# Kernel optimization log

Measured on AMD Instinct MI355X. Metric: run time of the kernel, lower is better.

The kernel has to match this reference:

```python
import jax, jax.numpy as jnp
import numpy as np
jax.config.update("jax_enable_x64", True)

T, C, F = 2048, 2048, 8192
f32 = jnp.float32
f64 = jnp.float64


def setup_inputs() -> dict:
    key = jax.random.key(0)
    ks = jax.random.split(key, 20)
    s = 0.02
    return {
        "x": jax.random.normal(ks[0], (T, C), f32),
        "att_shift": jnp.zeros((C,), f32),
        "wkv_state": jnp.zeros((2, C), f32),
        "ffn_shift": jnp.zeros((C,), f32),
        "ln1_w": jnp.ones((C,), f32),
        "ln1_b": jnp.zeros((C,), f32),
        "ln2_w": jnp.ones((C,), f32),
        "ln2_b": jnp.zeros((C,), f32),
        "time_mix_k": jax.random.uniform(ks[1], (C,), f32),
        "time_mix_v": jax.random.uniform(ks[2], (C,), f32),
        "time_mix_r": jax.random.uniform(ks[3], (C,), f32),
        "time_decay": jax.random.normal(ks[4], (C,), f32) * 0.5,
        "time_first": jax.random.normal(ks[5], (C,), f32) * 0.5,
        "att_key": jax.random.normal(ks[6], (C, C), f32) * s,
        "att_value": jax.random.normal(ks[7], (C, C), f32) * s,
        "att_receptance": jax.random.normal(ks[8], (C, C), f32) * s,
        "att_output": jax.random.normal(ks[9], (C, C), f32) * s,
        "ffn_time_mix_k": jax.random.uniform(ks[10], (C,), f32),
        "ffn_time_mix_r": jax.random.uniform(ks[11], (C,), f32),
        "ffn_key": jax.random.normal(ks[12], (F, C), f32) * s,
        "ffn_value": jax.random.normal(ks[13], (C, F), f32) * s,
        "ffn_receptance": jax.random.normal(ks[14], (C, C), f32) * s,
    }


def _ln(x, w, b):
    m = x.mean(-1, keepdims=True)
    v = x.var(-1, keepdims=True)
    return (x - m) * jax.lax.rsqrt(v + 1e-5) * w + b


def _wkv(time_decay, time_first, k, v, wkv_state):
    # faithful to wkv_mop: double-precision math, float32 state round-trip per step
    u = time_first.astype(f64)
    w = -jnp.exp(time_decay.astype(f64))
    ew = jnp.exp(w)

    def step(carry, kv_t):
        a, b = carry  # float32 states [C]
        k_t, v_t = kv_t
        kd = k_t.astype(f64)
        vd = v_t.astype(f64)
        e = jnp.exp(u + w + kd)
        y = (a + e * vd) / (b + e)
        kk = jnp.exp(kd)
        a2 = ((a + kk * vd) * ew).astype(f32)
        b2 = ((b + kk) * ew).astype(f32)
        return (a2, b2), y.astype(f32)

    _, y = jax.lax.scan(step, (wkv_state[0], wkv_state[1]), (k, v))
    return y  # [T, C]


def reference(x, att_shift, wkv_state, ffn_shift, ln1_w, ln1_b, ln2_w, ln2_b,
              time_mix_k, time_mix_v, time_mix_r, time_decay, time_first,
              att_key, att_value, att_receptance, att_output,
              ffn_time_mix_k, ffn_time_mix_r, ffn_key, ffn_value, ffn_receptance):
    # --- TimeMix (att) on rx = ln1(x); shiftamount=2 -> prev token of rx ---
    rx = _ln(x, ln1_w, ln1_b)                         # [T, C]
    xx = jnp.concatenate([att_shift[None, :], rx[:-1]], axis=0)
    xk = rx * time_mix_k + xx * (1.0 - time_mix_k)
    xv = rx * time_mix_v + xx * (1.0 - time_mix_v)
    xr = rx * time_mix_r + xx * (1.0 - time_mix_r)
    k = xk @ att_key.T                                # [T, C]
    v = xv @ att_value.T
    sr = jax.nn.sigmoid(xr @ att_receptance.T)
    y = _wkv(time_decay, time_first, k, v, wkv_state)
    x = x + (sr * y) @ att_output.T
    # --- ChannelMix (ffn) on fx = ln2(x); shift = prev token of fx ---
    fx = _ln(x, ln2_w, ln2_b)
    fxx = jnp.concatenate([ffn_shift[None, :], fx[:-1]], axis=0)
    fk = fx * ffn_time_mix_k + fxx * (1.0 - ffn_time_mix_k)
    fr = fx * ffn_time_mix_r + fxx * (1.0 - ffn_time_mix_r)
    kf = jnp.square(jax.nn.relu(fk @ ffn_key.T))      # [T, F]
    kv = kf @ ffn_value.T                             # [T, C]
    out = x + jax.nn.sigmoid(fr @ ffn_receptance.T) * kv
    return out
```

## Files before the change

kernel.cpp:

```cpp
#include <hip/hip_runtime.h>
#include <hip/hip_bf16.h>

typedef unsigned short u16;
typedef short bf16x8 __attribute__((ext_vector_type(8)));
typedef float f32x4 __attribute__((ext_vector_type(4)));

#define T_DIM 2048
#define C_DIM 2048
#define F_DIM 8192
#define WKV_L 32
#define WKV_P (T_DIM / WKV_L)

__device__ __forceinline__ u16 f2bf(float f) {
    unsigned int u = __float_as_uint(f);
    u += 0x7fff + ((u >> 16) & 1);
    return (u16)(u >> 16);
}

__device__ __forceinline__ void async16(const void* g, void* l) {
    __builtin_amdgcn_global_load_lds(
        (__attribute__((address_space(1))) const unsigned int*)g,
        (__attribute__((address_space(3))) unsigned int*)l, 16, 0, 0);
}

__global__ __launch_bounds__(256) void ln_mix3(
        const float* __restrict__ x, const float* __restrict__ sh,
        const float* __restrict__ w, const float* __restrict__ b,
        const float* __restrict__ mk, const float* __restrict__ mv,
        const float* __restrict__ mr,
        u16* __restrict__ xk, u16* __restrict__ xv, u16* __restrict__ xr) {
    __shared__ float red[16];
    const int t = blockIdx.x, tid = threadIdx.x;
    const float4* cr = (const float4*)(x + (size_t)t * C_DIM);
    float4 c0 = cr[tid * 2], c1 = cr[tid * 2 + 1];
    float s = c0.x + c0.y + c0.z + c0.w + c1.x + c1.y + c1.z + c1.w;
    float q = c0.x * c0.x + c0.y * c0.y + c0.z * c0.z + c0.w * c0.w
            + c1.x * c1.x + c1.y * c1.y + c1.z * c1.z + c1.w * c1.w;
    float4 p0, p1;
    float sp = 0.f, qp = 0.f;
    if (t > 0) {
        const float4* pr = (const float4*)(x + (size_t)(t - 1) * C_DIM);
        p0 = pr[tid * 2]; p1 = pr[tid * 2 + 1];
        sp = p0.x + p0.y + p0.z + p0.w + p1.x + p1.y + p1.z + p1.w;
        qp = p0.x * p0.x + p0.y * p0.y + p0.z * p0.z + p0.w * p0.w
           + p1.x * p1.x + p1.y * p1.y + p1.z * p1.z + p1.w * p1.w;
    } else {
        const float4* pr = (const float4*)sh;
        p0 = pr[tid * 2]; p1 = pr[tid * 2 + 1];
    }
    #pragma unroll
    for (int off = 32; off > 0; off >>= 1) {
        s += __shfl_down(s, off);   q += __shfl_down(q, off);
        sp += __shfl_down(sp, off); qp += __shfl_down(qp, off);
    }
    const int lane = tid & 63, wv = tid >> 6;
    if (lane == 0) { red[wv] = s; red[4 + wv] = q; red[8 + wv] = sp; red[12 + wv] = qp; }
    __syncthreads();
    if (tid == 0) {
        red[0] += red[1] + red[2] + red[3];
        red[4] += red[5] + red[6] + red[7];
        red[8] += red[9] + red[10] + red[11];
        red[12] += red[13] + red[14] + red[15];
    }
    __syncthreads();
    const float mc = red[0] * (1.f / C_DIM);
    const float ic = rsqrtf(red[4] * (1.f / C_DIM) - mc * mc + 1e-5f);
    const float mp = red[8] * (1.f / C_DIM);
    const float ip = rsqrtf(red[12] * (1.f / C_DIM) - mp * mp + 1e-5f);
    const float4* w4 = (const float4*)w;
    const float4* b4 = (const float4*)b;
    #pragma unroll
    for (int j = 0; j < 2; ++j) {
        const int i4 = tid * 2 + j;
        float4 cv = j ? c1 : c0, pv = j ? p1 : p0;
        float4 wv4 = w4[i4], bv = b4[i4];
        float4 cl, pl;
        cl.x = (cv.x - mc) * ic * wv4.x + bv.x;
        cl.y = (cv.y - mc) * ic * wv4.y + bv.y;
        cl.z = (cv.z - mc) * ic * wv4.z + bv.z;
        cl.w = (cv.w - mc) * ic * wv4.w + bv.w;
        if (t > 0) {
            pl.x = (pv.x - mp) * ip * wv4.x + bv.x;
            pl.y = (pv.y - mp) * ip * wv4.y + bv.y;
            pl.z = (pv.z - mp) * ip * wv4.z + bv.z;
            pl.w = (pv.w - mp) * ip * wv4.w + bv.w;
        } else pl = pv;
        const size_t o = (size_t)t * (C_DIM / 4) + i4;
        float4 m;
        ushort4 r;
        m = ((const float4*)mk)[i4];
        r.x = f2bf(cl.x * m.x + pl.x * (1.f - m.x));
        r.y = f2bf(cl.y * m.y + pl.y * (1.f - m.y));
        r.z = f2bf(cl.z * m.z + pl.z * (1.f - m.z));
        r.w = f2bf(cl.w * m.w + pl.w * (1.f - m.w));
        ((ushort4*)xk)[o] = r;
        m = ((const float4*)mv)[i4];
        r.x = f2bf(cl.x * m.x + pl.x * (1.f - m.x));
        r.y = f2bf(cl.y * m.y + pl.y * (1.f - m.y));
        r.z = f2bf(cl.z * m.z + pl.z * (1.f - m.z));
        r.w = f2bf(cl.w * m.w + pl.w * (1.f - m.w));
        ((ushort4*)xv)[o] = r;
        m = ((const float4*)mr)[i4];
        r.x = f2bf(cl.x * m.x + pl.x * (1.f - m.x));
        r.y = f2bf(cl.y * m.y + pl.y * (1.f - m.y));
        r.z = f2bf(cl.z * m.z + pl.z * (1.f - m.z));
        r.w = f2bf(cl.w * m.w + pl.w * (1.f - m.w));
        ((ushort4*)xr)[o] = r;
    }
}

__global__ __launch_bounds__(256) void ln_mix2(
        const float* __restrict__ x, const float* __restrict__ sh,
        const float* __restrict__ w, const float* __restrict__ b,
        const float* __restrict__ mk, const float* __restrict__ mr,
        u16* __restrict__ fk, u16* __restrict__ fr) {
    __shared__ float red[16];
    const int t = blockIdx.x, tid = threadIdx.x;
    const float4* cr = (const float4*)(x + (size_t)t * C_DIM);
    float4 c0 = cr[tid * 2], c1 = cr[tid * 2 + 1];
    float s = c0.x + c0.y + c0.z + c0.w + c1.x + c1.y + c1.z + c1.w;
    float q = c0.x * c0.x + c0.y * c0.y + c0.z * c0.z + c0.w * c0.w
            + c1.x * c1.x + c1.y * c1.y + c1.z * c1.z + c1.w * c1.w;
    float4 p0, p1;
    float sp = 0.f, qp = 0.f;
    if (t > 0) {
        const float4* pr = (const float4*)(x + (size_t)(t - 1) * C_DIM);
        p0 = pr[tid * 2]; p1 = pr[tid * 2 + 1];
        sp = p0.x + p0.y + p0.z + p0.w + p1.x + p1.y + p1.z + p1.w;
        qp = p0.x * p0.x + p0.y * p0.y + p0.z * p0.z + p0.w * p0.w
           + p1.x * p1.x + p1.y * p1.y + p1.z * p1.z + p1.w * p1.w;
    } else {
        const float4* pr = (const float4*)sh;
        p0 = pr[tid * 2]; p1 = pr[tid * 2 + 1];
    }
    #pragma unroll
    for (int off = 32; off > 0; off >>= 1) {
        s += __shfl_down(s, off);   q += __shfl_down(q, off);
        sp += __shfl_down(sp, off); qp += __shfl_down(qp, off);
    }
    const int lane = tid & 63, wv = tid >> 6;
    if (lane == 0) { red[wv] = s; red[4 + wv] = q; red[8 + wv] = sp; red[12 + wv] = qp; }
    __syncthreads();
    if (tid == 0) {
        red[0] += red[1] + red[2] + red[3];
        red[4] += red[5] + red[6] + red[7];
        red[8] += red[9] + red[10] + red[11];
        red[12] += red[13] + red[14] + red[15];
    }
    __syncthreads();
    const float mc = red[0] * (1.f / C_DIM);
    const float ic = rsqrtf(red[4] * (1.f / C_DIM) - mc * mc + 1e-5f);
    const float mp = red[8] * (1.f / C_DIM);
    const float ip = rsqrtf(red[12] * (1.f / C_DIM) - mp * mp + 1e-5f);
    const float4* w4 = (const float4*)w;
    const float4* b4 = (const float4*)b;
    #pragma unroll
    for (int j = 0; j < 2; ++j) {
        const int i4 = tid * 2 + j;
        float4 cv = j ? c1 : c0, pv = j ? p1 : p0;
        float4 wv4 = w4[i4], bv = b4[i4];
        float4 cl, pl;
        cl.x = (cv.x - mc) * ic * wv4.x + bv.x;
        cl.y = (cv.y - mc) * ic * wv4.y + bv.y;
        cl.z = (cv.z - mc) * ic * wv4.z + bv.z;
        cl.w = (cv.w - mc) * ic * wv4.w + bv.w;
        if (t > 0) {
            pl.x = (pv.x - mp) * ip * wv4.x + bv.x;
            pl.y = (pv.y - mp) * ip * wv4.y + bv.y;
            pl.z = (pv.z - mp) * ip * wv4.z + bv.z;
            pl.w = (pv.w - mp) * ip * wv4.w + bv.w;
        } else pl = pv;
        const size_t o = (size_t)t * (C_DIM / 4) + i4;
        float4 m;
        ushort4 r;
        m = ((const float4*)mk)[i4];
        r.x = f2bf(cl.x * m.x + pl.x * (1.f - m.x));
        r.y = f2bf(cl.y * m.y + pl.y * (1.f - m.y));
        r.z = f2bf(cl.z * m.z + pl.z * (1.f - m.z));
        r.w = f2bf(cl.w * m.w + pl.w * (1.f - m.w));
        ((ushort4*)fk)[o] = r;
        m = ((const float4*)mr)[i4];
        r.x = f2bf(cl.x * m.x + pl.x * (1.f - m.x));
        r.y = f2bf(cl.y * m.y + pl.y * (1.f - m.y));
        r.z = f2bf(cl.z * m.z + pl.z * (1.f - m.z));
        r.w = f2bf(cl.w * m.w + pl.w * (1.f - m.w));
        ((ushort4*)fr)[o] = r;
    }
}

__global__ __launch_bounds__(256) void cvt_bf16(const float* __restrict__ in,
                                                u16* __restrict__ out, int n8) {
    int i = blockIdx.x * 256 + threadIdx.x;
    const int stride = gridDim.x * 256;
    for (; i < n8; i += stride) {
        const float4* p = (const float4*)(in + (size_t)i * 8);
        float4 a = p[0], b = p[1];
        ushort4 lo, hi;
        lo.x = f2bf(a.x); lo.y = f2bf(a.y); lo.z = f2bf(a.z); lo.w = f2bf(a.w);
        hi.x = f2bf(b.x); hi.y = f2bf(b.y); hi.z = f2bf(b.z); hi.w = f2bf(b.w);
        ((ushort4*)out)[i * 2] = lo;
        ((ushort4*)out)[i * 2 + 1] = hi;
    }
}

__global__ __launch_bounds__(256) void cvt4_bf16(const float* __restrict__ i0,
                                                 const float* __restrict__ i1,
                                                 const float* __restrict__ i2,
                                                 const float* __restrict__ i3,
                                                 u16* __restrict__ out, int n8) {
    const int sel = blockIdx.y;
    const float* in = sel == 0 ? i0 : (sel == 1 ? i1 : (sel == 2 ? i2 : i3));
    u16* o = out + (size_t)sel * n8 * 8;
    int i = blockIdx.x * 256 + threadIdx.x;
    const int stride = gridDim.x * 256;
    for (; i < n8; i += stride) {
        const float4* p = (const float4*)(in + (size_t)i * 8);
        float4 a = p[0], b = p[1];
        ushort4 lo, hi;
        lo.x = f2bf(a.x); lo.y = f2bf(a.y); lo.z = f2bf(a.z); lo.w = f2bf(a.w);
        hi.x = f2bf(b.x); hi.y = f2bf(b.y); hi.z = f2bf(b.z); hi.w = f2bf(b.w);
        ((ushort4*)o)[i * 2] = lo;
        ((ushort4*)o)[i * 2 + 1] = hi;
    }
}

__global__ __launch_bounds__(256) void reduce4(const float* __restrict__ p0,
                                               const float* __restrict__ p1,
                                               const float* __restrict__ p2,
                                               const float* __restrict__ p3,
                                               float* __restrict__ o, int n4) {
    int i = blockIdx.x * 256 + threadIdx.x;
    const int stride = gridDim.x * 256;
    for (; i < n4; i += stride) {
        float4 a = ((const float4*)p0)[i], b = ((const float4*)p1)[i];
        float4 c = ((const float4*)p2)[i], d = ((const float4*)p3)[i];
        float4 r;
        r.x = a.x + b.x + c.x + d.x;
        r.y = a.y + b.y + c.y + d.y;
        r.z = a.z + b.z + c.z + d.z;
        r.w = a.w + b.w + c.w + d.w;
        ((float4*)o)[i] = r;
    }
}

__global__ __launch_bounds__(256) void wkv_part(const float* __restrict__ td,
                                                const float* __restrict__ k,
                                                const float* __restrict__ v,
                                                float* __restrict__ Ab,
                                                float* __restrict__ Bb) {
    const int idx = blockIdx.x * 256 + threadIdx.x;
    const int c = idx & (C_DIM - 1);
    const int p = idx >> 11;
    const float ew = expf(-expf(td[c]));
    float A = 0.f, B = 0.f;
    size_t o = (size_t)(p * WKV_L) * C_DIM + c;
    #pragma unroll 4
    for (int i = 0; i < WKV_L; ++i, o += C_DIM) {
        const float kk = expf(k[o]);
        A = (A + kk * v[o]) * ew;
        B = (B + kk) * ew;
    }
    Ab[p * C_DIM + c] = A;
    Bb[p * C_DIM + c] = B;
}

__global__ __launch_bounds__(256) void wkv_comb(const float* __restrict__ td,
                                                const float* __restrict__ st,
                                                const float* __restrict__ Ab,
                                                const float* __restrict__ Bb,
                                                float* __restrict__ Sa,
                                                float* __restrict__ Sb) {
    const int c = blockIdx.x * 256 + threadIdx.x;
    const float w = -expf(td[c]);
    const float dL = expf(w * (float)WKV_L);
    float a = st[c];
    float b = st[C_DIM + c];
    #pragma unroll 4
    for (int p = 0; p < WKV_P; ++p) {
        Sa[p * C_DIM + c] = a;
        Sb[p * C_DIM + c] = b;
        a = dL * a + Ab[p * C_DIM + c];
        b = dL * b + Bb[p * C_DIM + c];
    }
}

__global__ __launch_bounds__(256) void wkv_emit(const float* __restrict__ td,
                                                const float* __restrict__ tf,
                                                const float* __restrict__ k,
                                                const float* __restrict__ v,
                                                const float* __restrict__ r,
                                                const float* __restrict__ Sa,
                                                const float* __restrict__ Sb,
                                                u16* __restrict__ pout) {
    const int idx = blockIdx.x * 256 + threadIdx.x;
    const int c = idx & (C_DIM - 1);
    const int p = idx >> 11;
    const float u = tf[c];
    const float w = -expf(td[c]);
    const float ew = expf(w);
    float a = Sa[p * C_DIM + c];
    float b = Sb[p * C_DIM + c];
    size_t o = (size_t)(p * WKV_L) * C_DIM + c;
    #pragma unroll 2
    for (int i = 0; i < WKV_L; ++i, o += C_DIM) {
        const float kt = k[o], vt = v[o], rt = r[o];
        const float e = expf(u + w + kt);
        const float y = (a + e * vt) / (b + e);
        const float kk = expf(kt);
        a = (a + kk * vt) * ew;
        b = (b + kk) * ew;
        const float sr = 1.f / (1.f + expf(-rt));
        pout[o] = f2bf(sr * y);
    }
}

enum { EPI_F32 = 0, EPI_ADDX = 1, EPI_RELU2 = 2, EPI_SIGMULADD = 3 };

template <int EPI>
__global__ __launch_bounds__(256, 3) void gemm_bt(
        const u16* __restrict__ A, int lda, long a_zs,
        const u16* __restrict__ B, int ldb, long b_zs,
        long koff, int Kloop,
        void* __restrict__ outp, int ldo, long o_zs,
        const float* __restrict__ aux1, const float* __restrict__ aux2) {
    __shared__ u16 lds[3 * 8192];
    const int tid = threadIdx.x;
    const int l = tid & 63, w = tid >> 6;
    const int wr2 = w >> 1, wc2 = w & 1;

    const int gx = gridDim.x, gy = gridDim.y;
    const int nxy = gx * gy;
    const int flat = (blockIdx.z * gy + blockIdx.y) * gx + blockIdx.x;
    const int cpx = (nxy * gridDim.z) >> 3;
    const int swz = (flat & 7) * cpx + (flat >> 3);
    const int z = swz / nxy;
    const int rem = swz - z * nxy;
    const int bm = rem % gy;
    const int bn = rem / gy;

    const u16* Ag = A + (size_t)z * a_zs + (size_t)z * koff + (size_t)bm * 128 * lda;
    const u16* Bg = B + (size_t)z * b_zs + (size_t)z * koff + (size_t)bn * 128 * ldb;

    long gA[2], gB[2];
    int dA[2], dB[2];
    #pragma unroll
    for (int j = 0; j < 2; ++j) {
        const int off = j * 4096 + w * 1024 + l * 16;
        const int row = off >> 6;
        const int cb = (off & 63) ^ (((off >> 9) & 1) << 5);
        gA[j] = (long)row * lda + (cb >> 1);
        gB[j] = (long)row * ldb + (cb >> 1);
        dA[j] = j * 2048 + w * 512;
        dB[j] = 4096 + j * 2048 + w * 512;
    }

    int offA[4], offB[4];
    #pragma unroll
    for (int m = 0; m < 4; ++m) {
        const int lin = (wr2 * 64 + m * 16 + (l & 15)) * 64 + ((l >> 4) << 4);
        offA[m] = (lin ^ (((lin >> 9) & 1) << 5)) >> 1;
    }
    #pragma unroll
    for (int n = 0; n < 4; ++n) {
        const int lin = (wc2 * 64 + n * 16 + (l & 15)) * 64 + ((l >> 4) << 4);
        offB[n] = 4096 + ((lin ^ (((lin >> 9) & 1) << 5)) >> 1);
    }

    const f32x4 fz = {0.f, 0.f, 0.f, 0.f};
    f32x4 acc[4][4];
    #pragma unroll
    for (int m = 0; m < 4; ++m)
        #pragma unroll
        for (int n = 0; n < 4; ++n) acc[m][n] = fz;

    const int NT = Kloop >> 5;

    auto stage = [&](int kt, int sp) {
        const long ko = (long)kt << 5;
        const int sb = sp * 8192;
        async16(Ag + gA[0] + ko, &lds[sb + dA[0]]);
        async16(Ag + gA[1] + ko, &lds[sb + dA[1]]);
        async16(Bg + gB[0] + ko, &lds[sb + dB[0]]);
        async16(Bg + gB[1] + ko, &lds[sb + dB[1]]);
    };

    stage(0, 0);
    stage(1, 1);

    int sr = 0;
    for (int t = 0; t < NT; ++t) {
        asm volatile("s_waitcnt vmcnt(4)" ::: "memory");
        __builtin_amdgcn_s_barrier();
        __builtin_amdgcn_sched_barrier(0);
        {
            const int tp = (t + 2 < NT) ? t + 2 : NT - 1;
            const int sp = (sr == 0) ? 2 : sr - 1;
            stage(tp, sp);
        }
        const int sb = sr * 8192;
        bf16x8 af[4], bfv[4];
        #pragma unroll
        for (int m = 0; m < 4; ++m) af[m] = *(const bf16x8*)&lds[sb + offA[m]];
        #pragma unroll
        for (int n = 0; n < 4; ++n) bfv[n] = *(const bf16x8*)&lds[sb + offB[n]];
        __builtin_amdgcn_s_setprio(1);
        #pragma unroll
        for (int m = 0; m < 2; ++m)
            #pragma unroll
            for (int n = 0; n < 4; ++n)
                acc[m][n] = __builtin_amdgcn_mfma_f32_16x16x32_bf16(af[m], bfv[n], acc[m][n], 0, 0, 0);
        __builtin_amdgcn_s_setprio(0);
        __builtin_amdgcn_s_setprio(1);
        #pragma unroll
        for (int m = 2; m < 4; ++m)
            #pragma unroll
            for (int n = 0; n < 4; ++n)
                acc[m][n] = __builtin_amdgcn_mfma_f32_16x16x32_bf16(af[m], bfv[n], acc[m][n], 0, 0, 0);
        __builtin_amdgcn_s_setprio(0);
        sr = (sr == 2) ? 0 : sr + 1;
    }
    asm volatile("s_waitcnt vmcnt(0)" ::: "memory");

    const int r00 = bm * 128 + wr2 * 64 + ((l >> 4) << 2);
    const int c00 = bn * 128 + wc2 * 64 + (l & 15);
    #pragma unroll
    for (int m = 0; m < 4; ++m) {
        #pragma unroll
        for (int n = 0; n < 4; ++n) {
            #pragma unroll
            for (int j = 0; j < 4; ++j) {
                const int rr = r00 + m * 16 + j;
                const int cc = c00 + n * 16;
                const size_t o = (size_t)rr * ldo + cc;
                const float val = acc[m][n][j];
                if constexpr (EPI == EPI_F32) {
                    ((float*)outp)[(size_t)z * o_zs + o] = val;
                } else if constexpr (EPI == EPI_ADDX) {
                    ((float*)outp)[o] = aux1[o] + val;
                } else if constexpr (EPI == EPI_RELU2) {
                    const float tp2 = fmaxf(val, 0.f);
                    ((u16*)outp)[o] = f2bf(tp2 * tp2);
                } else {
                    const float sg = 1.f / (1.f + expf(-val));
                    ((float*)outp)[o] = aux1[o] + sg * aux2[o];
                }
            }
        }
    }
}

template <int EPI>
__global__ __launch_bounds__(512, 2) void gemm3s(
        const u16* __restrict__ A, int lda,
        const u16* __restrict__ B, int ldb,
        long koff, int Kloop,
        void* __restrict__ outp, int ldo, long o_zs) {
    __shared__ u16 lds[3 * 16384];
    const int tid = threadIdx.x;
    const int l = tid & 63, w = tid >> 6;
    const int wm = w >> 2, wn = w & 3;

    const int gx = gridDim.x, gy = gridDim.y;
    const int nxy = gx * gy;
    const int flat = (blockIdx.z * gy + blockIdx.y) * gx + blockIdx.x;
    const int cpx = (nxy * gridDim.z) >> 3;
    const int swzb = (flat & 7) * cpx + (flat >> 3);
    const int z = swzb / nxy;
    const int rem = swzb - z * nxy;
    const int bm = rem % gy;
    const int bn = rem / gy;

    const u16* Ag = A + (size_t)z * koff + (size_t)bm * 256 * lda;
    const u16* Bg = B + (size_t)z * koff + (size_t)bn * 256 * ldb;

    long srcA[2], srcB[2];
    int dstA[2], dstB[2];
    #pragma unroll
    for (int h = 0; h < 2; ++h) {
        const int off = h * 8192 + w * 1024 + l * 16;
        const int row = off >> 6;
        const int cbyte = (off & 63) ^ (((off >> 9) & 1) << 5);
        srcA[h] = (long)row * lda + (cbyte >> 1);
        srcB[h] = (long)row * ldb + (cbyte >> 1);
        dstA[h] = off >> 1;
        dstB[h] = 8192 + (off >> 1);
    }

    int offAL[4], offAH[4], offB[4];
    #pragma unroll
    for (int mi = 0; mi < 4; ++mi) {
        int row = wm * 128 + mi * 16 + (l & 15);
        int lin = row * 64 + ((l >> 4) << 4);
        offAL[mi] = (lin ^ (((lin >> 9) & 1) << 5)) >> 1;
        lin = (row + 64) * 64 + ((l >> 4) << 4);
        offAH[mi] = (lin ^ (((lin >> 9) & 1) << 5)) >> 1;
    }
    #pragma unroll
    for (int n = 0; n < 4; ++n) {
        const int row = wn * 64 + n * 16 + (l & 15);
        const int lin = row * 64 + ((l >> 4) << 4);
        offB[n] = 8192 + ((lin ^ (((lin >> 9) & 1) << 5)) >> 1);
    }

    const f32x4 fz = {0.f, 0.f, 0.f, 0.f};
    f32x4 acc[8][4];
    #pragma unroll
    for (int m = 0; m < 8; ++m)
        #pragma unroll
        for (int n = 0; n < 4; ++n) acc[m][n] = fz;

    const int NT = Kloop >> 5;

    auto stgA = [&](int kt, int buf, int h) {
        async16(Ag + srcA[h] + (long)kt * 32, &lds[buf * 16384 + dstA[h]]);
    };
    auto stgB = [&](int kt, int buf, int h) {
        async16(Bg + srcB[h] + (long)kt * 32, &lds[buf * 16384 + dstB[h]]);
    };

    stgA(0, 0, 0); stgA(0, 0, 1); stgB(0, 0, 0); stgB(0, 0, 1);
    stgA(1, 1, 0); stgA(1, 1, 1); stgB(1, 1, 0); stgB(1, 1, 1);
    asm volatile("s_waitcnt vmcnt(4)" ::: "memory");
    __builtin_amdgcn_s_barrier();

    bf16x8 aX[4], bX[4], aY[4], bY[4];
    #pragma unroll
    for (int mi = 0; mi < 4; ++mi) aX[mi] = *(const bf16x8*)&lds[offAL[mi]];
    #pragma unroll
    for (int n = 0; n < 4; ++n) bX[n] = *(const bf16x8*)&lds[offB[n]];

    auto tile = [&](int kt, bf16x8 (&aC)[4], bf16x8 (&bbC)[4],
                    bf16x8 (&aN)[4], bf16x8 (&bbN)[4]) {
        const int cb = (kt % 3) * 16384;
        const int nb = ((kt + 1) % 3) * 16384;
        const int tb = (kt + 2) % 3;
        const int ksrc = (kt + 2 < NT) ? kt + 2 : NT - 1;
        bf16x8 aH[4];
        #pragma unroll
        for (int mi = 0; mi < 4; ++mi) aH[mi] = *(const bf16x8*)&lds[cb + offAH[mi]];
        stgA(ksrc, tb, 0); stgA(ksrc, tb, 1);
        __builtin_amdgcn_s_barrier();
        asm volatile("s_waitcnt lgkmcnt(4)" ::: "memory");
        __builtin_amdgcn_sched_barrier(0);
        __builtin_amdgcn_s_setprio(1);
        #pragma unroll
        for (int mi = 0; mi < 4; ++mi)
            #pragma unroll
            for (int n = 0; n < 4; ++n)
                acc[mi][n] = __builtin_amdgcn_mfma_f32_16x16x32_bf16(aC[mi], bbC[n], acc[mi][n], 0, 0, 0);
        __builtin_amdgcn_s_setprio(0);
        asm volatile("s_waitcnt vmcnt(2)" ::: "memory");
        __builtin_amdgcn_s_barrier();
        #pragma unroll
        for (int mi = 0; mi < 4; ++mi) aN[mi] = *(const bf16x8*)&lds[nb + offAL[mi]];
        #pragma unroll
        for (int n = 0; n < 4; ++n) bbN[n] = *(const bf16x8*)&lds[nb + offB[n]];
        stgB(ksrc, tb, 0); stgB(ksrc, tb, 1);
        __builtin_amdgcn_s_barrier();
        asm volatile("s_waitcnt lgkmcnt(8)" ::: "memory");
        __builtin_amdgcn_sched_barrier(0);
        __builtin_amdgcn_s_setprio(1);
        #pragma unroll
        for (int mi = 0; mi < 4; ++mi)
            #pragma unroll
            for (int n = 0; n < 4; ++n)
                acc[4 + mi][n] = __builtin_amdgcn_mfma_f32_16x16x32_bf16(aH[mi], bbC[n], acc[4 + mi][n], 0, 0, 0);
        __builtin_amdgcn_s_setprio(0);
        __builtin_amdgcn_s_barrier();
    };

    for (int kt = 0; kt < NT; kt += 2) {
        tile(kt, aX, bX, aY, bY);
        tile(kt + 1, aY, bY, aX, bX);
    }
    asm volatile("s_waitcnt vmcnt(0)" ::: "memory");

    const int r00 = bm * 256 + wm * 128 + ((l >> 4) << 2);
    const int c00 = bn * 256 + wn * 64 + (l & 15);
    #pragma unroll
    for (int m = 0; m < 8; ++m) {
        #pragma unroll
        for (int n = 0; n < 4; ++n) {
            #pragma unroll
            for (int j = 0; j < 4; ++j) {
                const int rr = r00 + m * 16 + j;
                const int cc = c00 + n * 16;
                const size_t o = (size_t)rr * ldo + cc;
                const float val = acc[m][n][j];
                if constexpr (EPI == EPI_F32) {
                    ((float*)outp)[(size_t)z * o_zs + o] = val;
                } else {
                    const float tp2 = fmaxf(val, 0.f);
                    ((u16*)outp)[o] = f2bf(tp2 * tp2);
                }
            }
        }
    }
}

extern "C" void kernel_launch(void* const* d_in, const int* in_sizes, int n_in,
                              void* d_out, int out_size, void* d_ws, size_t ws_size,
                              hipStream_t stream) {
    const float* x         = (const float*)d_in[0];
    const float* att_shift = (const float*)d_in[1];
    const float* wkv_state = (const float*)d_in[2];
    const float* ffn_shift = (const float*)d_in[3];
    const float* ln1w = (const float*)d_in[4];
    const float* ln1b = (const float*)d_in[5];
    const float* ln2w = (const float*)d_in[6];
    const float* ln2b = (const float*)d_in[7];
    const float* tmk  = (const float*)d_in[8];
    const float* tmv  = (const float*)d_in[9];
    const float* tmr  = (const float*)d_in[10];
    const float* td   = (const float*)d_in[11];
    const float* tf   = (const float*)d_in[12];
    const float* Wk   = (const float*)d_in[13];
    const float* Wv   = (const float*)d_in[14];
    const float* Wr   = (const float*)d_in[15];
    const float* Wo   = (const float*)d_in[16];
    const float* ftmk = (const float*)d_in[17];
    const float* ftmr = (const float*)d_in[18];
    const float* Wfk  = (const float*)d_in[19];
    const float* Wfv  = (const float*)d_in[20];
    const float* Wfr  = (const float*)d_in[21];
    float* out = (float*)d_out;

    char* ws = (char*)d_ws;
    const size_t MB = 1ull << 20;
    float* rx0 = (float*)(ws + 0);
    u16*   xk  = (u16*)(ws + 16 * MB);
    u16*   xv  = (u16*)(ws + 24 * MB);
    u16*   xr  = (u16*)(ws + 32 * MB);
    float* kb  = (float*)(ws + 40 * MB);
    float* vb  = (float*)(ws + 56 * MB);
    float* rb  = (float*)(ws + 72 * MB);
    u16*   pb  = (u16*)(ws + 88 * MB);
    float* x1  = (float*)(ws + 96 * MB);
    u16*   kf  = (u16*)(ws + 112 * MB);
    u16*   Wb  = (u16*)(ws + 144 * MB);
    float* wAb = (float*)(ws + 112 * MB);
    float* wBb = (float*)(ws + 112 * MB + 512 * 1024);
    float* wSa = (float*)(ws + 113 * MB);
    float* wSb = (float*)(ws + 113 * MB + 512 * 1024);
    float* fvp = (float*)(ws + 32 * MB);

    const int T = T_DIM, C = C_DIM, F = F_DIM;
    const dim3 blk(256), blk5(512);

    ln_mix3<<<T, blk, 0, stream>>>(x, att_shift, ln1w, ln1b, tmk, tmv, tmr, xk, xv, xr);

    cvt4_bf16<<<dim3(1024, 4), blk, 0, stream>>>(Wk, Wv, Wr, Wo, Wb, C * C / 8);
    gemm_bt<EPI_F32><<<dim3(C / 128, T / 128, 3), blk, 0, stream>>>(
        xk, C, (long)T * C, Wb, C, (long)C * C, 0, C,
        kb, C, (long)T * C, nullptr, nullptr);

    wkv_part<<<(C * WKV_P) / 256, blk, 0, stream>>>(td, kb, vb, wAb, wBb);
    wkv_comb<<<C / 256, blk, 0, stream>>>(td, wkv_state, wAb, wBb, wSa, wSb);
    wkv_emit<<<(C * WKV_P) / 256, blk, 0, stream>>>(td, tf, kb, vb, rb, wSa, wSb, pb);

    gemm_bt<EPI_ADDX><<<dim3(C / 128, T / 128, 1), blk, 0, stream>>>(
        pb, C, 0, Wb + 3 * (size_t)C * C, C, 0, 0, C, x1, C, 0, x, nullptr);

    ln_mix2<<<T, blk, 0, stream>>>(x1, ffn_shift, ln2w, ln2b, ftmk, ftmr, xk, xv);

    cvt_bf16<<<2048, blk, 0, stream>>>(Wfk, Wb, F * C / 8);
    gemm3s<EPI_RELU2><<<dim3(F / 256, T / 256, 1), blk5, 0, stream>>>(
        xk, C, Wb, C, 0, C, kf, F, 0);

    cvt_bf16<<<2048, blk, 0, stream>>>(Wfv, Wb, C * F / 8);
    gemm3s<EPI_F32><<<dim3(C / 256, T / 256, 4), blk5, 0, stream>>>(
        kf, F, Wb, F, 2048, 2048, fvp, C, (long)T * C);
    reduce4<<<2048, blk, 0, stream>>>(fvp, fvp + (size_t)T * C, fvp + 2 * (size_t)T * C,
                                      fvp + 3 * (size_t)T * C, rx0, T * C / 4);

    cvt_bf16<<<2048, blk, 0, stream>>>(Wfr, Wb, C * C / 8);
    gemm_bt<EPI_SIGMULADD><<<dim3(C / 128, T / 128, 1), blk, 0, stream>>>(
        xv, C, 0, Wb, C, 0, 0, C, out, C, 0, x1, rx0);
}
```

Measured before the change: 391.2 us.

## Split-K the square GEMMs and deepen FFN GEMM pipeline to four stages

The output projection and FFN receptance GEMMs (256 tiles each at 128x128) are now split-K into two halves. This doubles the block count so the GPU's many CUs are better filled. The partial results are written to fp32 scratch and then combined in new elementwise kernels (residual add, and sigmoid-multiply-add). Separately, the big FFN GEMM kernel goes from a 3-buffer to a 4-buffer LDS ring with one more tile prefetched, which hides more global load latency. The cost is extra scratch traffic, two more launches, and 128KB of LDS per block, which may limit occupancy with two blocks per CU.

```diff
diff --git a/kernel.cpp b/kernel.cpp
--- a/kernel.cpp
+++ b/kernel.cpp
@@ -243,6 +243,43 @@
     }
 }
 
+__global__ __launch_bounds__(256) void comb_add(const float* __restrict__ p0,
+                                                const float* __restrict__ p1,
+                                                const float* __restrict__ xin,
+                                                float* __restrict__ o, int n4) {
+    int i = blockIdx.x * 256 + threadIdx.x;
+    const int stride = gridDim.x * 256;
+    for (; i < n4; i += stride) {
+        float4 a = ((const float4*)p0)[i], b = ((const float4*)p1)[i];
+        float4 c = ((const float4*)xin)[i];
+        float4 r;
+        r.x = a.x + b.x + c.x;
+        r.y = a.y + b.y + c.y;
+        r.z = a.z + b.z + c.z;
+        r.w = a.w + b.w + c.w;
+        ((float4*)o)[i] = r;
+    }
+}
+
+__global__ __launch_bounds__(256) void comb_sig(const float* __restrict__ p0,
+                                                const float* __restrict__ p1,
+                                                const float* __restrict__ x1,
+                                                const float* __restrict__ kv,
+                                                float* __restrict__ o, int n4) {
+    int i = blockIdx.x * 256 + threadIdx.x;
+    const int stride = gridDim.x * 256;
+    for (; i < n4; i += stride) {
+        float4 a = ((const float4*)p0)[i], b = ((const float4*)p1)[i];
+        float4 c = ((const float4*)x1)[i], d = ((const float4*)kv)[i];
+        float4 r;
+        r.x = c.x + d.x / (1.f + expf(-(a.x + b.x)));
+        r.y = c.y + d.y / (1.f + expf(-(a.y + b.y)));
+        r.z = c.z + d.z / (1.f + expf(-(a.z + b.z)));
+        r.w = c.w + d.w / (1.f + expf(-(a.w + b.w)));
+        ((float4*)o)[i] = r;
+    }
+}
+
 __global__ __launch_bounds__(256) void wkv_part(const float* __restrict__ td,
                                                 const float* __restrict__ k,
                                                 const float* __restrict__ v,
@@ -450,12 +487,12 @@
 }
 
 template <int EPI>
-__global__ __launch_bounds__(512, 2) void gemm3s(
+__global__ __launch_bounds__(512, 2) void gemm4s(
         const u16* __restrict__ A, int lda,
         const u16* __restrict__ B, int ldb,
         long koff, int Kloop,
         void* __restrict__ outp, int ldo, long o_zs) {
-    __shared__ u16 lds[3 * 16384];
+    __shared__ u16 lds[4 * 16384];
     const int tid = threadIdx.x;
     const int l = tid & 63, w = tid >> 6;
     const int wm = w >> 2, wn = w & 3;
@@ -520,7 +557,8 @@
 
     stgA(0, 0, 0); stgA(0, 0, 1); stgB(0, 0, 0); stgB(0, 0, 1);
     stgA(1, 1, 0); stgA(1, 1, 1); stgB(1, 1, 0); stgB(1, 1, 1);
-    asm volatile("s_waitcnt vmcnt(4)" ::: "memory");
+    stgA(2, 2, 0); stgA(2, 2, 1); stgB(2, 2, 0); stgB(2, 2, 1);
+    asm volatile("s_waitcnt vmcnt(8)" ::: "memory");
     __builtin_amdgcn_s_barrier();
 
     bf16x8 aX[4], bX[4], aY[4], bY[4];
@@ -531,10 +569,10 @@
 
     auto tile = [&](int kt, bf16x8 (&aC)[4], bf16x8 (&bbC)[4],
                     bf16x8 (&aN)[4], bf16x8 (&bbN)[4]) {
-        const int cb = (kt % 3) * 16384;
-        const int nb = ((kt + 1) % 3) * 16384;
-        const int tb = (kt + 2) % 3;
-        const int ksrc = (kt + 2 < NT) ? kt + 2 : NT - 1;
+        const int cb = (kt & 3) * 16384;
+        const int nb = ((kt + 1) & 3) * 16384;
+        const int tb = (kt + 3) & 3;
+        const int ksrc = (kt + 3 < NT) ? kt + 3 : NT - 1;
         bf16x8 aH[4];
         #pragma unroll
         for (int mi = 0; mi < 4; ++mi) aH[mi] = *(const bf16x8*)&lds[cb + offAH[mi]];
@@ -549,7 +587,7 @@
             for (int n = 0; n < 4; ++n)
                 acc[mi][n] = __builtin_amdgcn_mfma_f32_16x16x32_bf16(aC[mi], bbC[n], acc[mi][n], 0, 0, 0);
         __builtin_amdgcn_s_setprio(0);
-        asm volatile("s_waitcnt vmcnt(2)" ::: "memory");
+        asm volatile("s_waitcnt vmcnt(6)" ::: "memory");
         __builtin_amdgcn_s_barrier();
         #pragma unroll
         for (int mi = 0; mi < 4; ++mi) aN[mi] = *(const bf16x8*)&lds[nb + offAL[mi]];
@@ -642,7 +680,9 @@
     float* wBb = (float*)(ws + 112 * MB + 512 * 1024);
     float* wSa = (float*)(ws + 113 * MB);
     float* wSb = (float*)(ws + 113 * MB + 512 * 1024);
+    float* aop = (float*)(ws + 40 * MB);
     float* fvp = (float*)(ws + 32 * MB);
+    float* rcp = (float*)(ws + 40 * MB);
 
     const int T = T_DIM, C = C_DIM, F = F_DIM;
     const dim3 blk(256), blk5(512);
@@ -658,22 +698,25 @@
     wkv_comb<<<C / 256, blk, 0, stream>>>(td, wkv_state, wAb, wBb, wSa, wSb);
     wkv_emit<<<(C * WKV_P) / 256, blk, 0, stream>>>(td, tf, kb, vb, rb, wSa, wSb, pb);
 
-    gemm_bt<EPI_ADDX><<<dim3(C / 128, T / 128, 1), blk, 0, stream>>>(
-        pb, C, 0, Wb + 3 * (size_t)C * C, C, 0, 0, C, x1, C, 0, x, nullptr);
+    gemm_bt<EPI_F32><<<dim3(C / 128, T / 128, 2), blk, 0, stream>>>(
+        pb, C, 0, Wb + 3 * (size_t)C * C, C, 0, 1024, 1024,
+        aop, C, (long)T * C, nullptr, nullptr);
+    comb_add<<<2048, blk, 0, stream>>>(aop, aop + (size_t)T * C, x, x1, T * C / 4);
 
     ln_mix2<<<T, blk, 0, stream>>>(x1, ffn_shift, ln2w, ln2b, ftmk, ftmr, xk, xv);
 
     cvt_bf16<<<2048, blk, 0, stream>>>(Wfk, Wb, F * C / 8);
-    gemm3s<EPI_RELU2><<<dim3(F / 256, T / 256, 1), blk5, 0, stream>>>(
+    gemm4s<EPI_RELU2><<<dim3(F / 256, T / 256, 1), blk5, 0, stream>>>(
         xk, C, Wb, C, 0, C, kf, F, 0);
 
     cvt_bf16<<<2048, blk, 0, stream>>>(Wfv, Wb, C * F / 8);
-    gemm3s<EPI_F32><<<dim3(C / 256, T / 256, 4), blk5, 0, stream>>>(
+    gemm4s<EPI_F32><<<dim3(C / 256, T / 256, 4), blk5, 0, stream>>>(
         kf, F, Wb, F, 2048, 2048, fvp, C, (long)T * C);
     reduce4<<<2048, blk, 0, stream>>>(fvp, fvp + (size_t)T * C, fvp + 2 * (size_t)T * C,
                                       fvp + 3 * (size_t)T * C, rx0, T * C / 4);
 
     cvt_bf16<<<2048, blk, 0, stream>>>(Wfr, Wb, C * C / 8);
-    gemm_bt<EPI_SIGMULADD><<<dim3(C / 128, T / 128, 1), blk, 0, stream>>>(
-        xv, C, 0, Wb, C, 0, 0, C, out, C, 0, x1, rx0);
-}
+    gemm_bt<EPI_F32><<<dim3(C / 128, T / 128, 2), blk, 0, stream>>>(
+        xv, C, 0, Wb, C, 0, 1024, 1024, rcp, C, (long)T * C, nullptr, nullptr);
+    comb_sig<<<2048, blk, 0, stream>>>(rcp, rcp + (size_t)T * C, x1, rx0, out, T * C / 4);
+}
```

Measured after the change: 396.2 us. About the same (+1.3%).

## Deepen FFN GEMM pipeline to four LDS stages and fuse split-K reduce

Applied to the files above, without the earlier changes.

The large FFN GEMM kernel moves from a 3-stage to a 4-stage LDS ring buffer. It prefetches three K-tiles ahead, with vmcnt waits adjusted to match. Separately, the standalone reduce4 kernel that summed the four split-K partials is removed, and the final receptance GEMM epilogue now reads and sums those four partials directly. This saves one launch plus a full write and read of a T×C buffer. The cost is 128KB of LDS per block, which may limit occupancy.

```diff
diff --git a/kernel.cpp b/kernel.cpp
--- a/kernel.cpp
+++ b/kernel.cpp
@@ -224,25 +224,6 @@
     }
 }
 
-__global__ __launch_bounds__(256) void reduce4(const float* __restrict__ p0,
-                                               const float* __restrict__ p1,
-                                               const float* __restrict__ p2,
-                                               const float* __restrict__ p3,
-                                               float* __restrict__ o, int n4) {
-    int i = blockIdx.x * 256 + threadIdx.x;
-    const int stride = gridDim.x * 256;
-    for (; i < n4; i += stride) {
-        float4 a = ((const float4*)p0)[i], b = ((const float4*)p1)[i];
-        float4 c = ((const float4*)p2)[i], d = ((const float4*)p3)[i];
-        float4 r;
-        r.x = a.x + b.x + c.x + d.x;
-        r.y = a.y + b.y + c.y + d.y;
-        r.z = a.z + b.z + c.z + d.z;
-        r.w = a.w + b.w + c.w + d.w;
-        ((float4*)o)[i] = r;
-    }
-}
-
 __global__ __launch_bounds__(256) void wkv_part(const float* __restrict__ td,
                                                 const float* __restrict__ k,
                                                 const float* __restrict__ v,
@@ -314,7 +295,7 @@
     }
 }
 
-enum { EPI_F32 = 0, EPI_ADDX = 1, EPI_RELU2 = 2, EPI_SIGMULADD = 3 };
+enum { EPI_F32 = 0, EPI_ADDX = 1, EPI_RELU2 = 2, EPI_SIGMULADD = 3, EPI_SIGMULADD4 = 4 };
 
 template <int EPI>
 __global__ __launch_bounds__(256, 3) void gemm_bt(
@@ -440,9 +421,16 @@
                 } else if constexpr (EPI == EPI_RELU2) {
                     const float tp2 = fmaxf(val, 0.f);
                     ((u16*)outp)[o] = f2bf(tp2 * tp2);
-                } else {
+                } else if constexpr (EPI == EPI_SIGMULADD) {
                     const float sg = 1.f / (1.f + expf(-val));
                     ((float*)outp)[o] = aux1[o] + sg * aux2[o];
+                } else {
+                    const float kv = aux2[o]
+                                   + aux2[o + (size_t)T_DIM * C_DIM]
+                                   + aux2[o + 2 * (size_t)T_DIM * C_DIM]
+                                   + aux2[o + 3 * (size_t)T_DIM * C_DIM];
+                    const float sg = 1.f / (1.f + expf(-val));
+                    ((float*)outp)[o] = aux1[o] + sg * kv;
                 }
             }
         }
@@ -450,12 +438,12 @@
 }
 
 template <int EPI>
-__global__ __launch_bounds__(512, 2) void gemm3s(
+__global__ __launch_bounds__(512, 2) void gemm4s(
         const u16* __restrict__ A, int lda,
         const u16* __restrict__ B, int ldb,
         long koff, int Kloop,
         void* __restrict__ outp, int ldo, long o_zs) {
-    __shared__ u16 lds[3 * 16384];
+    __shared__ u16 lds[4 * 16384];
     const int tid = threadIdx.x;
     const int l = tid & 63, w = tid >> 6;
     const int wm = w >> 2, wn = w & 3;
@@ -520,7 +508,8 @@
 
     stgA(0, 0, 0); stgA(0, 0, 1); stgB(0, 0, 0); stgB(0, 0, 1);
     stgA(1, 1, 0); stgA(1, 1, 1); stgB(1, 1, 0); stgB(1, 1, 1);
-    asm volatile("s_waitcnt vmcnt(4)" ::: "memory");
+    stgA(2, 2, 0); stgA(2, 2, 1); stgB(2, 2, 0); stgB(2, 2, 1);
+    asm volatile("s_waitcnt vmcnt(8)" ::: "memory");
     __builtin_amdgcn_s_barrier();
 
     bf16x8 aX[4], bX[4], aY[4], bY[4];
@@ -531,10 +520,10 @@
 
     auto tile = [&](int kt, bf16x8 (&aC)[4], bf16x8 (&bbC)[4],
                     bf16x8 (&aN)[4], bf16x8 (&bbN)[4]) {
-        const int cb = (kt % 3) * 16384;
-        const int nb = ((kt + 1) % 3) * 16384;
-        const int tb = (kt + 2) % 3;
-        const int ksrc = (kt + 2 < NT) ? kt + 2 : NT - 1;
+        const int cb = (kt & 3) * 16384;
+        const int nb = ((kt + 1) & 3) * 16384;
+        const int tb = (kt + 3) & 3;
+        const int ksrc = (kt + 3 < NT) ? kt + 3 : NT - 1;
         bf16x8 aH[4];
         #pragma unroll
         for (int mi = 0; mi < 4; ++mi) aH[mi] = *(const bf16x8*)&lds[cb + offAH[mi]];
@@ -549,7 +538,7 @@
             for (int n = 0; n < 4; ++n)
                 acc[mi][n] = __builtin_amdgcn_mfma_f32_16x16x32_bf16(aC[mi], bbC[n], acc[mi][n], 0, 0, 0);
         __builtin_amdgcn_s_setprio(0);
-        asm volatile("s_waitcnt vmcnt(2)" ::: "memory");
+        asm volatile("s_waitcnt vmcnt(6)" ::: "memory");
         __builtin_amdgcn_s_barrier();
         #pragma unroll
         for (int mi = 0; mi < 4; ++mi) aN[mi] = *(const bf16x8*)&lds[nb + offAL[mi]];
@@ -627,7 +616,6 @@
 
     char* ws = (char*)d_ws;
     const size_t MB = 1ull << 20;
-    float* rx0 = (float*)(ws + 0);
     u16*   xk  = (u16*)(ws + 16 * MB);
     u16*   xv  = (u16*)(ws + 24 * MB);
     u16*   xr  = (u16*)(ws + 32 * MB);
@@ -664,16 +652,14 @@
     ln_mix2<<<T, blk, 0, stream>>>(x1, ffn_shift, ln2w, ln2b, ftmk, ftmr, xk, xv);
 
     cvt_bf16<<<2048, blk, 0, stream>>>(Wfk, Wb, F * C / 8);
-    gemm3s<EPI_RELU2><<<dim3(F / 256, T / 256, 1), blk5, 0, stream>>>(
+    gemm4s<EPI_RELU2><<<dim3(F / 256, T / 256, 1), blk5, 0, stream>>>(
         xk, C, Wb, C, 0, C, kf, F, 0);
 
     cvt_bf16<<<2048, blk, 0, stream>>>(Wfv, Wb, C * F / 8);
-    gemm3s<EPI_F32><<<dim3(C / 256, T / 256, 4), blk5, 0, stream>>>(
+    gemm4s<EPI_F32><<<dim3(C / 256, T / 256, 4), blk5, 0, stream>>>(
         kf, F, Wb, F, 2048, 2048, fvp, C, (long)T * C);
-    reduce4<<<2048, blk, 0, stream>>>(fvp, fvp + (size_t)T * C, fvp + 2 * (size_t)T * C,
-                                      fvp + 3 * (size_t)T * C, rx0, T * C / 4);
 
     cvt_bf16<<<2048, blk, 0, stream>>>(Wfr, Wb, C * C / 8);
-    gemm_bt<EPI_SIGMULADD><<<dim3(C / 128, T / 128, 1), blk, 0, stream>>>(
-        xv, C, 0, Wb, C, 0, 0, C, out, C, 0, x1, rx0);
-}
+    gemm_bt<EPI_SIGMULADD4><<<dim3(C / 128, T / 128, 1), blk, 0, stream>>>(
+        xv, C, 0, Wb, C, 0, 0, C, out, C, 0, x1, fvp);
+}
```

New measurement: 381.6 us. 1.03x faster.
